# Performance work log

Hardware: AMD Instinct MI355X
Metric: run time of the kernel (lower is better)

## Reference

```python
import jax, jax.numpy as jnp
import numpy as np

K = (0.3, 0.3, 0.4)   # args.args_k_0..2
EPS = 1e-8


def squash(v, axis=-1):
    norm = jnp.linalg.norm(v, axis=axis, keepdims=True)
    scale = norm ** 2 / (1.0 + norm ** 2) / (norm + EPS)
    return scale * v


def setup_inputs() -> dict:
    key = jax.random.key(0)
    kx, kw = jax.random.split(key)
    B, IN, DIN, OUT, DOUT = 128, 4608, 8, 10, 16
    x = jax.random.normal(kx, (B, IN, DIN), dtype=jnp.float32)
    weight = 0.1 * jax.random.normal(kw, (OUT, IN, DOUT, DIN), dtype=jnp.float32)
    return {"x": x, "weight": weight}


def reference(x, weight):
    # x: [B, I, Din], weight: [O, I, Dout, Din]
    # x_hat[b,o,i,d] = sum_k weight[o,i,d,k] * x[b,i,k]
    x_hat = jnp.einsum('oidk,bik->boid', weight, x)  # [B, O, I, Dout]
    x_hat_d = jax.lax.stop_gradient(x_hat)
    B, O, I, D = x_hat.shape
    b = jnp.zeros((B, O, I), dtype=x.dtype)
    feats = []
    for it in range(3):
        c = jax.nn.softmax(b, axis=1)[..., None]          # [B, O, I, 1], softmax over out caps
        if it == 2:
            out = squash(jnp.sum(c * x_hat, axis=-2, keepdims=True))      # [B, O, 1, D]
        else:
            out = squash(jnp.sum(c * x_hat_d, axis=-2, keepdims=True))    # [B, O, 1, D]
            b = b + jnp.sum(out * x_hat_d, axis=-1)                       # agreement update
        feats.append(out * K[it])
    # stack -> [3, B, O, 1, D]; squeeze caps-sum axis; sum over iterations
    outputs = jnp.sum(jnp.squeeze(jnp.stack(feats), axis=-2), axis=0)     # [B, O, D]
    return outputs.reshape(B, O, 4, 4)
```

## Files before the change

### kernel.cpp

```cpp
#include <hip/hip_runtime.h>

#define B_    128
#define I_    4608
#define O_    10
#define D_    16
#define NCHUNKS 2304
#define NIB   64
#define CPB   36
#define CHH   5120
#define PSET  20480

typedef _Float16 f16x2 __attribute__((ext_vector_type(2)));
typedef _Float16 f16x4 __attribute__((ext_vector_type(4)));
typedef _Float16 f16x8 __attribute__((ext_vector_type(8)));
typedef float    f32x4 __attribute__((ext_vector_type(4)));
typedef __fp16   pk16x2 __attribute__((ext_vector_type(2)));
typedef unsigned int uint2v __attribute__((ext_vector_type(2)));

__device__ __forceinline__ f16x4 pack4(float a, float b, float c, float d) {
    union { f16x4 v; pk16x2 p[2]; } u;
    u.p[0] = __builtin_amdgcn_cvt_pkrtz(a, b);
    u.p[1] = __builtin_amdgcn_cvt_pkrtz(c, d);
    return u.v;
}
__device__ __forceinline__ f16x2 splat_h2(float a) {
    union { f16x2 v; pk16x2 p; } u;
    u.p = __builtin_amdgcn_cvt_pkrtz(a, a);
    return u.v;
}

__global__ __launch_bounds__(256)
void prep_kernel(const float* __restrict__ w, _Float16* __restrict__ pw)
{
    __shared__ float wch[2560];
    const int c = blockIdx.x, t = threadIdx.x;
#pragma unroll
    for (int o = 0; o < O_; ++o)
        wch[o * 256 + t] = w[(long)o * (I_ * 128) + (long)c * 256 + t];
    __syncthreads();

    _Float16* dst = pw + (long)c * CHH;
#pragma unroll
    for (int kk = 0; kk < 5; ++kk) {
        const int sidx = t + kk * 256;
        const int hg   = sidx & 1;
        const int lane = (sidx >> 1) & 63;
        const int pi   = sidx >> 7;
        const int p    = pi % 5;
        const int img  = pi / 5;
        const int r = lane & 15, g = lane >> 4;
        const int o = 2 * p + hg;
        f16x4 val;
        if (img == 1) {
            const float4 gg = *(const float4*)&wch[o * 256 + (g & 1) * 128 + r * 8 + (g >> 1) * 4];
            val = pack4(gg.x, gg.y, gg.z, gg.w);
        } else {
            const int bofs = o * 256 + ((r >> 2) & 1) * 128 + (r >> 3) * 4 + (r & 3);
            val = pack4(wch[bofs + (g * 4 + 0) * 8], wch[bofs + (g * 4 + 1) * 8],
                        wch[bofs + (g * 4 + 2) * 8], wch[bofs + (g * 4 + 3) * 8]);
        }
        *(f16x4*)(dst + (long)sidx * 4) = val;
    }
}

template<int MODE>
__global__ __launch_bounds__(512, 2)
void pass_kernel(const float* __restrict__ x,
                 const _Float16* __restrict__ pw,
                 const float* __restrict__ v,
                 float* __restrict__ parts)
{
    __shared__ float red[4 * 5120];

    const int tid  = threadIdx.x;
    const int lane = tid & 63;
    const int wv   = tid >> 6;
    const int bl   = lane & 15;
    const int g    = lane >> 4;
    const int u    = blockIdx.x;
    const int xcd  = u & 7, s = u >> 3;
    const int ib   = xcd * 8 + (s & 7);
    const int bg   = s >> 3;
    const int c0   = ib * CPB;
    const int cend = c0 + CPB;
    const int iloc = g & 1, kq = g >> 1;
    const int b0   = bg * 32 + bl;

    f16x4 vf[2][O_];
    if (MODE == 1) {
#pragma unroll
        for (int tile = 0; tile < 2; ++tile)
#pragma unroll
            for (int o = 0; o < O_; ++o) {
                const float4 vv = *(const float4*)(v + ((long)(b0 + tile * 16) * O_ + o) * D_ + g * 4);
                vf[tile][o] = pack4(vv.x, vv.y, vv.z, vv.w);
            }
    }

    f32x4 S[2][O_];
#pragma unroll
    for (int tile = 0; tile < 2; ++tile)
#pragma unroll
        for (int o = 0; o < O_; ++o) S[tile][o] = (f32x4)(0.f);

    const long lofs = (long)lane * 8;
    auto fragp = [&](int c, int img, int p) {
        return (const f16x8*)(pw + (long)c * CHH + img * 2560 + p * 512 + lofs);
    };
    auto xp = [&](int c, int tile) {
        return (const float4*)(x + ((long)(b0 + tile * 16) * I_ + 2 * c + iloc) * 8 + kq * 4);
    };

    int c = c0 + wv;
    f16x8 f0[5], f1[5];
    float4 xqC[2], xqN[2];
    if (MODE == 1) {
#pragma unroll
        for (int p = 0; p < 5; ++p) f0[p] = *fragp(c, 0, p);
    }
#pragma unroll
    for (int p = 0; p < 5; ++p) f1[p] = *fragp(c, 1, p);
    xqC[0] = *xp(c, 0); xqC[1] = *xp(c, 1);

#pragma unroll
    for (int t5 = 0; t5 < 5; ++t5) {
        const bool valid = (c < cend);
        int cn = c + 8; if (cn > NCHUNKS - 1) cn = NCHUNKS - 1;
        if (valid) {
            xqN[0] = *xp(cn, 0); xqN[1] = *xp(cn, 1);

            float cs[2][O_];
            if (MODE == 1) {
#pragma unroll
                for (int tile = 0; tile < 2; ++tile)
#pragma unroll
                    for (int p = 0; p < 5; ++p) {
                        f16x4 ae, ao;
                        ae[0]=f0[p][0]; ae[1]=f0[p][1]; ae[2]=f0[p][2]; ae[3]=f0[p][3];
                        ao[0]=f0[p][4]; ao[1]=f0[p][5]; ao[2]=f0[p][6]; ao[3]=f0[p][7];
                        const f32x4 ua = __builtin_amdgcn_mfma_f32_16x16x16f16(ae, vf[tile][2*p],   (f32x4)(0.f), 0, 0, 0);
                        const f32x4 ub = __builtin_amdgcn_mfma_f32_16x16x16f16(ao, vf[tile][2*p+1], (f32x4)(0.f), 0, 0, 0);
                        const float4 xq = xqC[tile];
                        float d0 = ua[0] * xq.x; d0 = fmaf(ua[1], xq.y, d0);
                        d0 = fmaf(ua[2], xq.z, d0); d0 = fmaf(ua[3], xq.w, d0);
                        float d1 = ub[0] * xq.x; d1 = fmaf(ub[1], xq.y, d1);
                        d1 = fmaf(ub[2], xq.z, d1); d1 = fmaf(ub[3], xq.w, d1);
                        cs[tile][2*p] = d0; cs[tile][2*p+1] = d1;
                    }
#pragma unroll
                for (int p = 0; p < 5; ++p) f0[p] = *fragp(cn, 0, p);
#pragma unroll
                for (int tile = 0; tile < 2; ++tile) {
                    float ssum = 0.f;
#pragma unroll
                    for (int o = 0; o < O_; ++o) {
                        const unsigned int tt = __float_as_uint(cs[tile][o]);
                        const uint2v sw = __builtin_amdgcn_permlane32_swap(tt, tt, false, false);
                        const float e = __expf(__uint_as_float(sw[0]) + __uint_as_float(sw[1]));
                        cs[tile][o] = e; ssum += e;
                    }
                    const float inv = 1.f / ssum;
#pragma unroll
                    for (int o = 0; o < O_; ++o) cs[tile][o] *= inv;
                }
            }

            union F4 { f16x4 v; f16x2 h[2]; };
            F4 xh[2];
            xh[0].v = pack4(xqC[0].x, xqC[0].y, xqC[0].z, xqC[0].w);
            xh[1].v = pack4(xqC[1].x, xqC[1].y, xqC[1].z, xqC[1].w);
#pragma unroll
            for (int p = 0; p < 5; ++p) {
                f16x4 pe, po;
                pe[0]=f1[p][0]; pe[1]=f1[p][1]; pe[2]=f1[p][2]; pe[3]=f1[p][3];
                po[0]=f1[p][4]; po[1]=f1[p][5]; po[2]=f1[p][6]; po[3]=f1[p][7];
#pragma unroll
                for (int tile = 0; tile < 2; ++tile) {
                    F4 ye, yo;
                    if (MODE == 0) { ye = xh[tile]; yo = xh[tile]; }
                    else {
                        const f16x2 ce = splat_h2(cs[tile][2*p]);
                        const f16x2 co = splat_h2(cs[tile][2*p+1]);
                        ye.h[0] = xh[tile].h[0] * ce; ye.h[1] = xh[tile].h[1] * ce;
                        yo.h[0] = xh[tile].h[0] * co; yo.h[1] = xh[tile].h[1] * co;
                    }
                    S[tile][2*p]   = __builtin_amdgcn_mfma_f32_16x16x16f16(pe, ye.v, S[tile][2*p],   0, 0, 0);
                    S[tile][2*p+1] = __builtin_amdgcn_mfma_f32_16x16x16f16(po, yo.v, S[tile][2*p+1], 0, 0, 0);
                }
            }
#pragma unroll
            for (int p = 0; p < 5; ++p) f1[p] = *fragp(cn, 1, p);
            xqC[0] = xqN[0]; xqC[1] = xqN[1];
        }
        c += 8;
    }

    auto slot = [&](int w, int tile, int o) {
        return &red[w * 5120 + (tile * O_ + o) * 256 + lane * 4];
    };
#define TREE_WR(WSRC, WDST)                                                 \
    if (wv >= WSRC) {                                                       \
        _Pragma("unroll") for (int tile = 0; tile < 2; ++tile)              \
        _Pragma("unroll") for (int o = 0; o < O_; ++o)                      \
            *(f32x4*)slot(wv - WSRC, tile, o) = S[tile][o];                 \
    }                                                                       \
    __syncthreads();                                                        \
    if (wv < WSRC) {                                                        \
        _Pragma("unroll") for (int tile = 0; tile < 2; ++tile)              \
        _Pragma("unroll") for (int o = 0; o < O_; ++o)                      \
            S[tile][o] += *(f32x4*)slot(wv, tile, o);                       \
    }                                                                       \
    __syncthreads();

    TREE_WR(4, )
    TREE_WR(2, )
    TREE_WR(1, )
#undef TREE_WR

    if (wv == 0) {
#pragma unroll
        for (int tile = 0; tile < 2; ++tile)
#pragma unroll
            for (int o = 0; o < O_; ++o) {
                float* pp = parts + (long)ib * PSET
                          + ((long)(b0 + tile * 16) * O_ + o) * D_ + g * 4;
                *(f32x4*)pp = S[tile][o];
            }
    }
}

__global__ __launch_bounds__(256)
void reduce_squash(const float* __restrict__ parts, float* __restrict__ v_buf,
                   float* __restrict__ out, float kscale, float pre, int mode)
{
    __shared__ float red2[4][16];
    const int tid  = threadIdx.x;
    const int lane = tid & 63;
    const int wv   = tid >> 6;
    const int g2   = blockIdx.x;
    const int pg   = tid >> 4;
    const int d    = tid & 15;

    float s = 0.f;
#pragma unroll
    for (int k = 0; k < 4; ++k)
        s += parts[(long)(pg * 4 + k) * PSET + g2 * D_ + d];

    s += __shfl_xor(s, 16);
    s += __shfl_xor(s, 32);
    if (lane < 16) red2[wv][lane] = s;
    __syncthreads();

    if (tid < 16) {
        float tot = (red2[0][tid] + red2[1][tid]) + (red2[2][tid] + red2[3][tid]);
        tot *= pre;
        float n2 = tot * tot;
        n2 += __shfl_xor(n2, 1);
        n2 += __shfl_xor(n2, 2);
        n2 += __shfl_xor(n2, 4);
        n2 += __shfl_xor(n2, 8);
        const float n     = sqrtf(n2);
        const float scale = n2 / ((1.f + n2) * (n + 1e-8f));
        const float o_    = scale * tot;
        const int idx = g2 * D_ + tid;
        if (mode == 0)      { v_buf[idx] = o_;  out[idx]  = kscale * o_; }
        else if (mode == 1) { v_buf[idx] += o_; out[idx] += kscale * o_; }
        else                {                   out[idx] += kscale * o_; }
    }
}

extern "C" void kernel_launch(void* const* d_in, const int* in_sizes, int n_in,
                              void* d_out, int out_size, void* d_ws, size_t ws_size,
                              hipStream_t stream)
{
    const float* x = (const float*)d_in[0];
    const float* w = (const float*)d_in[1];
    float* out   = (float*)d_out;
    float* parts = (float*)d_ws;
    float* v_buf = parts + (long)NIB * PSET;
    _Float16* pw = (_Float16*)(v_buf + B_ * O_ * D_);

    prep_kernel<<<NCHUNKS, 256, 0, stream>>>(w, pw);

    pass_kernel<0><<<256, 512, 0, stream>>>(x, pw, v_buf, parts);
    reduce_squash<<<1280, 256, 0, stream>>>(parts, v_buf, out, 0.3f, 0.1f, 0);

    pass_kernel<1><<<256, 512, 0, stream>>>(x, pw, v_buf, parts);
    reduce_squash<<<1280, 256, 0, stream>>>(parts, v_buf, out, 0.3f, 1.0f, 1);

    pass_kernel<1><<<256, 512, 0, stream>>>(x, pw, v_buf, parts);
    reduce_squash<<<1280, 256, 0, stream>>>(parts, v_buf, out, 0.4f, 1.0f, 2);
}
```

Before: 72.40 us.

## Halve per-block batch tile to double grid size and raise occupancy

Each pass-kernel block now handles 16 batch rows instead of 32, with one tile instead of two. The grid doubles from 256 to 512 blocks, launch bounds ask for 4 blocks per CU, and the shared reduction buffer is halved. The aim is to cut register and LDS pressure and expose more parallelism and latency hiding. The cost is that each weight fragment loaded from global memory is reused for half as many batch rows, so weight traffic doubles. The tree reduction now writes only from waves in [WSRC, 2*WSRC).

```diff
diff --git a/kernel.cpp b/kernel.cpp
--- a/kernel.cpp
+++ b/kernel.cpp
@@ -64,13 +64,13 @@
 }
 
 template<int MODE>
-__global__ __launch_bounds__(512, 2)
+__global__ __launch_bounds__(512, 4)
 void pass_kernel(const float* __restrict__ x,
                  const _Float16* __restrict__ pw,
                  const float* __restrict__ v,
                  float* __restrict__ parts)
 {
-    __shared__ float red[4 * 5120];
+    __shared__ float red[4 * 2560];
 
     const int tid  = threadIdx.x;
     const int lane = tid & 63;
@@ -84,148 +84,129 @@
     const int c0   = ib * CPB;
     const int cend = c0 + CPB;
     const int iloc = g & 1, kq = g >> 1;
-    const int b0   = bg * 32 + bl;
-
-    f16x4 vf[2][O_];
+    const int b0   = bg * 16 + bl;
+
+    f16x4 vf[O_];
     if (MODE == 1) {
 #pragma unroll
-        for (int tile = 0; tile < 2; ++tile)
-#pragma unroll
-            for (int o = 0; o < O_; ++o) {
-                const float4 vv = *(const float4*)(v + ((long)(b0 + tile * 16) * O_ + o) * D_ + g * 4);
-                vf[tile][o] = pack4(vv.x, vv.y, vv.z, vv.w);
-            }
-    }
-
-    f32x4 S[2][O_];
-#pragma unroll
-    for (int tile = 0; tile < 2; ++tile)
-#pragma unroll
-        for (int o = 0; o < O_; ++o) S[tile][o] = (f32x4)(0.f);
+        for (int o = 0; o < O_; ++o) {
+            const float4 vv = *(const float4*)(v + ((long)b0 * O_ + o) * D_ + g * 4);
+            vf[o] = pack4(vv.x, vv.y, vv.z, vv.w);
+        }
+    }
+
+    f32x4 S[O_];
+#pragma unroll
+    for (int o = 0; o < O_; ++o) S[o] = (f32x4)(0.f);
 
     const long lofs = (long)lane * 8;
     auto fragp = [&](int c, int img, int p) {
         return (const f16x8*)(pw + (long)c * CHH + img * 2560 + p * 512 + lofs);
     };
-    auto xp = [&](int c, int tile) {
-        return (const float4*)(x + ((long)(b0 + tile * 16) * I_ + 2 * c + iloc) * 8 + kq * 4);
+    auto xp = [&](int c) {
+        return (const float4*)(x + ((long)b0 * I_ + 2 * c + iloc) * 8 + kq * 4);
     };
 
     int c = c0 + wv;
     f16x8 f0[5], f1[5];
-    float4 xqC[2], xqN[2];
+    float4 xqC, xqN;
     if (MODE == 1) {
 #pragma unroll
         for (int p = 0; p < 5; ++p) f0[p] = *fragp(c, 0, p);
     }
 #pragma unroll
     for (int p = 0; p < 5; ++p) f1[p] = *fragp(c, 1, p);
-    xqC[0] = *xp(c, 0); xqC[1] = *xp(c, 1);
+    xqC = *xp(c);
 
 #pragma unroll
     for (int t5 = 0; t5 < 5; ++t5) {
         const bool valid = (c < cend);
         int cn = c + 8; if (cn > NCHUNKS - 1) cn = NCHUNKS - 1;
         if (valid) {
-            xqN[0] = *xp(cn, 0); xqN[1] = *xp(cn, 1);
-
-            float cs[2][O_];
+            xqN = *xp(cn);
+
+            float cs[O_];
             if (MODE == 1) {
 #pragma unroll
-                for (int tile = 0; tile < 2; ++tile)
-#pragma unroll
-                    for (int p = 0; p < 5; ++p) {
-                        f16x4 ae, ao;
-                        ae[0]=f0[p][0]; ae[1]=f0[p][1]; ae[2]=f0[p][2]; ae[3]=f0[p][3];
-                        ao[0]=f0[p][4]; ao[1]=f0[p][5]; ao[2]=f0[p][6]; ao[3]=f0[p][7];
-                        const f32x4 ua = __builtin_amdgcn_mfma_f32_16x16x16f16(ae, vf[tile][2*p],   (f32x4)(0.f), 0, 0, 0);
-                        const f32x4 ub = __builtin_amdgcn_mfma_f32_16x16x16f16(ao, vf[tile][2*p+1], (f32x4)(0.f), 0, 0, 0);
-                        const float4 xq = xqC[tile];
-                        float d0 = ua[0] * xq.x; d0 = fmaf(ua[1], xq.y, d0);
-                        d0 = fmaf(ua[2], xq.z, d0); d0 = fmaf(ua[3], xq.w, d0);
-                        float d1 = ub[0] * xq.x; d1 = fmaf(ub[1], xq.y, d1);
-                        d1 = fmaf(ub[2], xq.z, d1); d1 = fmaf(ub[3], xq.w, d1);
-                        cs[tile][2*p] = d0; cs[tile][2*p+1] = d1;
-                    }
+                for (int p = 0; p < 5; ++p) {
+                    f16x4 ae, ao;
+                    ae[0]=f0[p][0]; ae[1]=f0[p][1]; ae[2]=f0[p][2]; ae[3]=f0[p][3];
+                    ao[0]=f0[p][4]; ao[1]=f0[p][5]; ao[2]=f0[p][6]; ao[3]=f0[p][7];
+                    const f32x4 ua = __builtin_amdgcn_mfma_f32_16x16x16f16(ae, vf[2*p],   (f32x4)(0.f), 0, 0, 0);
+                    const f32x4 ub = __builtin_amdgcn_mfma_f32_16x16x16f16(ao, vf[2*p+1], (f32x4)(0.f), 0, 0, 0);
+                    float d0 = ua[0] * xqC.x; d0 = fmaf(ua[1], xqC.y, d0);
+                    d0 = fmaf(ua[2], xqC.z, d0); d0 = fmaf(ua[3], xqC.w, d0);
+                    float d1 = ub[0] * xqC.x; d1 = fmaf(ub[1], xqC.y, d1);
+                    d1 = fmaf(ub[2], xqC.z, d1); d1 = fmaf(ub[3], xqC.w, d1);
+                    cs[2*p] = d0; cs[2*p+1] = d1;
+                }
 #pragma unroll
                 for (int p = 0; p < 5; ++p) f0[p] = *fragp(cn, 0, p);
-#pragma unroll
-                for (int tile = 0; tile < 2; ++tile) {
-                    float ssum = 0.f;
-#pragma unroll
-                    for (int o = 0; o < O_; ++o) {
-                        const unsigned int tt = __float_as_uint(cs[tile][o]);
-                        const uint2v sw = __builtin_amdgcn_permlane32_swap(tt, tt, false, false);
-                        const float e = __expf(__uint_as_float(sw[0]) + __uint_as_float(sw[1]));
-                        cs[tile][o] = e; ssum += e;
-                    }
-                    const float inv = 1.f / ssum;
-#pragma unroll
-                    for (int o = 0; o < O_; ++o) cs[tile][o] *= inv;
+                float ssum = 0.f;
+#pragma unroll
+                for (int o = 0; o < O_; ++o) {
+                    const unsigned int tt = __float_as_uint(cs[o]);
+                    const uint2v sw = __builtin_amdgcn_permlane32_swap(tt, tt, false, false);
+                    const float e = __expf(__uint_as_float(sw[0]) + __uint_as_float(sw[1]));
+                    cs[o] = e; ssum += e;
                 }
+                const float inv = 1.f / ssum;
+#pragma unroll
+                for (int o = 0; o < O_; ++o) cs[o] *= inv;
             }
 
             union F4 { f16x4 v; f16x2 h[2]; };
-            F4 xh[2];
-            xh[0].v = pack4(xqC[0].x, xqC[0].y, xqC[0].z, xqC[0].w);
-            xh[1].v = pack4(xqC[1].x, xqC[1].y, xqC[1].z, xqC[1].w);
+            F4 xh;
+            xh.v = pack4(xqC.x, xqC.y, xqC.z, xqC.w);
 #pragma unroll
             for (int p = 0; p < 5; ++p) {
                 f16x4 pe, po;
                 pe[0]=f1[p][0]; pe[1]=f1[p][1]; pe[2]=f1[p][2]; pe[3]=f1[p][3];
                 po[0]=f1[p][4]; po[1]=f1[p][5]; po[2]=f1[p][6]; po[3]=f1[p][7];
-#pragma unroll
-                for (int tile = 0; tile < 2; ++tile) {
-                    F4 ye, yo;
-                    if (MODE == 0) { ye = xh[tile]; yo = xh[tile]; }
-                    else {
-                        const f16x2 ce = splat_h2(cs[tile][2*p]);
-                        const f16x2 co = splat_h2(cs[tile][2*p+1]);
-                        ye.h[0] = xh[tile].h[0] * ce; ye.h[1] = xh[tile].h[1] * ce;
-                        yo.h[0] = xh[tile].h[0] * co; yo.h[1] = xh[tile].h[1] * co;
-                    }
-                    S[tile][2*p]   = __builtin_amdgcn_mfma_f32_16x16x16f16(pe, ye.v, S[tile][2*p],   0, 0, 0);
-                    S[tile][2*p+1] = __builtin_amdgcn_mfma_f32_16x16x16f16(po, yo.v, S[tile][2*p+1], 0, 0, 0);
+                F4 ye, yo;
+                if (MODE == 0) { ye = xh; yo = xh; }
+                else {
+                    const f16x2 ce = splat_h2(cs[2*p]);
+                    const f16x2 co = splat_h2(cs[2*p+1]);
+                    ye.h[0] = xh.h[0] * ce; ye.h[1] = xh.h[1] * ce;
+                    yo.h[0] = xh.h[0] * co; yo.h[1] = xh.h[1] * co;
                 }
+                S[2*p]   = __builtin_amdgcn_mfma_f32_16x16x16f16(pe, ye.v, S[2*p],   0, 0, 0);
+                S[2*p+1] = __builtin_amdgcn_mfma_f32_16x16x16f16(po, yo.v, S[2*p+1], 0, 0, 0);
             }
 #pragma unroll
             for (int p = 0; p < 5; ++p) f1[p] = *fragp(cn, 1, p);
-            xqC[0] = xqN[0]; xqC[1] = xqN[1];
+            xqC = xqN;
         }
         c += 8;
     }
 
-    auto slot = [&](int w, int tile, int o) {
-        return &red[w * 5120 + (tile * O_ + o) * 256 + lane * 4];
+    auto slot = [&](int w, int o) {
+        return &red[w * 2560 + o * 256 + lane * 4];
     };
-#define TREE_WR(WSRC, WDST)                                                 \
-    if (wv >= WSRC) {                                                       \
-        _Pragma("unroll") for (int tile = 0; tile < 2; ++tile)              \
+#define TREE_WR(WSRC)                                                       \
+    if (wv >= WSRC && wv < 2 * WSRC) {                                      \
         _Pragma("unroll") for (int o = 0; o < O_; ++o)                      \
-            *(f32x4*)slot(wv - WSRC, tile, o) = S[tile][o];                 \
+            *(f32x4*)slot(wv - WSRC, o) = S[o];                             \
     }                                                                       \
     __syncthreads();                                                        \
     if (wv < WSRC) {                                                        \
-        _Pragma("unroll") for (int tile = 0; tile < 2; ++tile)              \
         _Pragma("unroll") for (int o = 0; o < O_; ++o)                      \
-            S[tile][o] += *(f32x4*)slot(wv, tile, o);                       \
+            S[o] += *(f32x4*)slot(wv, o);                                   \
     }                                                                       \
     __syncthreads();
 
-    TREE_WR(4, )
-    TREE_WR(2, )
-    TREE_WR(1, )
+    TREE_WR(4)
+    TREE_WR(2)
+    TREE_WR(1)
 #undef TREE_WR
 
     if (wv == 0) {
 #pragma unroll
-        for (int tile = 0; tile < 2; ++tile)
-#pragma unroll
-            for (int o = 0; o < O_; ++o) {
-                float* pp = parts + (long)ib * PSET
-                          + ((long)(b0 + tile * 16) * O_ + o) * D_ + g * 4;
-                *(f32x4*)pp = S[tile][o];
-            }
+        for (int o = 0; o < O_; ++o) {
+            float* pp = parts + (long)ib * PSET + ((long)b0 * O_ + o) * D_ + g * 4;
+            *(f32x4*)pp = S[o];
+        }
     }
 }
 
@@ -282,12 +263,12 @@
 
     prep_kernel<<<NCHUNKS, 256, 0, stream>>>(w, pw);
 
-    pass_kernel<0><<<256, 512, 0, stream>>>(x, pw, v_buf, parts);
+    pass_kernel<0><<<512, 512, 0, stream>>>(x, pw, v_buf, parts);
     reduce_squash<<<1280, 256, 0, stream>>>(parts, v_buf, out, 0.3f, 0.1f, 0);
 
-    pass_kernel<1><<<256, 512, 0, stream>>>(x, pw, v_buf, parts);
+    pass_kernel<1><<<512, 512, 0, stream>>>(x, pw, v_buf, parts);
     reduce_squash<<<1280, 256, 0, stream>>>(parts, v_buf, out, 0.3f, 1.0f, 1);
 
-    pass_kernel<1><<<256, 512, 0, stream>>>(x, pw, v_buf, parts);
+    pass_kernel<1><<<512, 512, 0, stream>>>(x, pw, v_buf, parts);
     reduce_squash<<<1280, 256, 0, stream>>>(parts, v_buf, out, 0.4f, 1.0f, 2);
 }
```

After: 71.22 us. No clear change (-1.6%).
